# Performance work log

Measured on AMD Instinct MI355X. Metric: run time of the kernel, lower is better.

The kernel has to match this reference:

```python
import jax, jax.numpy as jnp
import numpy as np

B, S, E, H = 2, 2048, 1024, 16
DH = E // H  # 64


def setup_inputs() -> dict:
    key = jax.random.key(0)
    ks = jax.random.split(key, 10)
    scale = 1.0 / np.sqrt(E)
    x = jax.random.normal(ks[0], (B, S, E), dtype=jnp.float32)
    mask = jax.random.randint(ks[1], (B, S), 0, 2, dtype=jnp.int32)
    # per-head Q/K/V projections stacked: [H, E, DH] (x @ W, torch Linear transposed)
    wq = jax.random.normal(ks[2], (H, E, DH), dtype=jnp.float32) * scale
    wk = jax.random.normal(ks[3], (H, E, DH), dtype=jnp.float32) * scale
    wv = jax.random.normal(ks[4], (H, E, DH), dtype=jnp.float32) * scale
    bq = jax.random.normal(ks[5], (H, DH), dtype=jnp.float32) * scale
    bk = jax.random.normal(ks[6], (H, DH), dtype=jnp.float32) * scale
    bv = jax.random.normal(ks[7], (H, DH), dtype=jnp.float32) * scale
    wo = jax.random.normal(ks[8], (E, E), dtype=jnp.float32) * scale
    bo = jax.random.normal(ks[9], (E,), dtype=jnp.float32) * scale
    return {"x": x, "mask": mask, "wq": wq, "bq": bq, "wk": wk, "bk": bk,
            "wv": wv, "bv": bv, "wo": wo, "bo": bo}


def reference(x, mask, wq, bq, wk, bk, wv, bv, wo, bo):
    # q,k,v: [B, H, S, DH]
    q = jnp.einsum('bse,hed->bhsd', x, wq) + bq[None, :, None, :]
    k = jnp.einsum('bse,hed->bhsd', x, wk) + bk[None, :, None, :]
    v = jnp.einsum('bse,hed->bhsd', x, wv) + bv[None, :, None, :]
    scores = jnp.einsum('bhsd,bhtd->bhst', q, k) / np.sqrt(DH)
    # padding mask on key axis: mask==0 -> -1e9 (as in masked_fill)
    scores = jnp.where(mask[:, None, None, :] == 0, jnp.float32(-1e9), scores)
    attn = jax.nn.softmax(scores, axis=-1)
    o = jnp.einsum('bhst,bhtd->bhsd', attn, v)
    # concat heads -> [B, S, E], then output projection
    o = o.transpose(0, 2, 1, 3).reshape(B, S, E)
    return o @ wo + bo
```

## Files before the change

kernel.cpp:

```cpp
#include <hip/hip_runtime.h>
#include <hip/hip_bf16.h>
#include <math.h>

#define Bsz 2
#define Ssz 2048
#define Esz 1024
#define Hsz 16
#define DHsz 64

typedef __bf16 bf16_t;
typedef __attribute__((ext_vector_type(8))) __bf16 bf16x8;
typedef __attribute__((ext_vector_type(4))) float f32x4;

typedef unsigned int u32;
typedef const __attribute__((address_space(1))) u32* gptr_t;
typedef __attribute__((address_space(3))) u32* lptr_t;

#if __has_builtin(__builtin_amdgcn_exp2f)
#define EXP2F(x) __builtin_amdgcn_exp2f(x)
#else
#define EXP2F(x) __expf((x)*0.69314718f)
#endif

__device__ __forceinline__ bf16_t to_bf16(float f) {
  union { float f; unsigned u; } v; v.f = f;
  unsigned r = (v.u + 0x7FFF + ((v.u >> 16) & 1)) >> 16;
  union { unsigned short s; bf16_t b; } o; o.s = (unsigned short)r;
  return o.b;
}

__device__ __forceinline__ unsigned pack2_rtz(float a, float b) {
#if __has_builtin(__builtin_amdgcn_perm)
  return __builtin_amdgcn_perm(__float_as_uint(b), __float_as_uint(a), 0x07060302u);
#else
  return (__float_as_uint(a) >> 16) | (__float_as_uint(b) & 0xFFFF0000u);
#endif
}

__device__ __forceinline__ unsigned pack2(float a, float b) {
  union { float f; unsigned u; } x, y; x.f = a; y.f = b;
  unsigned ra = (x.u + 0x7FFF + ((x.u >> 16) & 1)) >> 16;
  unsigned rb = (y.u + 0x7FFF + ((y.u >> 16) & 1)) >> 16;
  return ra | (rb << 16);
}

__device__ __forceinline__ f32x4 mfma16(bf16x8 a, bf16x8 b, f32x4 c) {
  return __builtin_amdgcn_mfma_f32_16x16x32_bf16(a, b, c, 0, 0, 0);
}

__device__ __forceinline__ void gload16(void* lds, const void* g) {
  __builtin_amdgcn_global_load_lds((gptr_t)g, (lptr_t)lds, 16, 0, 0);
}

#define PREP_CAST 4096
#define PREP_MASK 4112
__global__ __launch_bounds__(256) void prep(
    const float* __restrict__ x, const int* __restrict__ mask,
    const float* __restrict__ wq, const float* __restrict__ wk,
    const float* __restrict__ wv, const float* __restrict__ wo,
    bf16_t* __restrict__ xb, bf16_t* __restrict__ mb,
    bf16_t* __restrict__ wAll, bf16_t* __restrict__ wAllV, bf16_t* __restrict__ woT) {
  __shared__ bf16_t lT[64 * 72];
  const int bid = blockIdx.x, t = threadIdx.x;
  if (bid < PREP_CAST) {
    const int i = bid * 256 + t;
    float4 v = ((const float4*)x)[i];
    uint2 o; o.x = pack2(v.x, v.y); o.y = pack2(v.z, v.w);
    ((uint2*)xb)[i] = o;
  } else if (bid < PREP_MASK) {
    const int i = (bid - PREP_CAST) * 256 + t;
    mb[i] = to_bf16(mask[i] ? 1.0f : 0.0f);
  } else {
    const int t2 = bid - PREP_MASK;
    const int et = t2 & 15, h = (t2 >> 4) & 15, z = t2 >> 8;
    const float* src; int srcLD; bf16_t* dst;
    if (z == 0)      { src = wq + ((size_t)h * Esz + et * 64) * DHsz; srcLD = DHsz; dst = wAll  + (size_t)(h * 64) * Esz; }
    else if (z == 1) { src = wk + ((size_t)h * Esz + et * 64) * DHsz; srcLD = DHsz; dst = wAll  + (size_t)(1024 + h * 64) * Esz; }
    else if (z == 2) { src = wv + ((size_t)h * Esz + et * 64) * DHsz; srcLD = DHsz; dst = wAllV + (size_t)(h * 64) * Esz; }
    else             { src = wo + (size_t)(et * 64) * Esz + h * 64;   srcLD = Esz;  dst = woT   + (size_t)(h * 64) * Esz; }
#pragma unroll
    for (int rr = 0; rr < 4; rr++) {
      int er = rr * 16 + (t >> 4);
      int dc = (t & 15) * 4;
      float4 v = *(const float4*)&src[(size_t)er * srcLD + dc];
      lT[(dc + 0) * 72 + er] = to_bf16(v.x);
      lT[(dc + 1) * 72 + er] = to_bf16(v.y);
      lT[(dc + 2) * 72 + er] = to_bf16(v.z);
      lT[(dc + 3) * 72 + er] = to_bf16(v.w);
    }
    __syncthreads();
#pragma unroll
    for (int rr = 0; rr < 2; rr++) {
      int d = rr * 32 + (t >> 3);
      int e8 = (t & 7) * 8;
      bf16x8 o = *(const bf16x8*)&lT[d * 72 + e8];
      *(bf16x8*)&dst[(size_t)d * Esz + et * 64 + e8] = o;
    }
  }
}

template <int TM, int TN>
__device__ __forceinline__ void gemm_core(
    const bf16_t* __restrict__ Ab, const bf16_t* __restrict__ Bb, int K,
    bf16_t* lA, bf16_t* lB, f32x4 (&acc)[TM / 32][TN / 32]) {
  const int tid = threadIdx.x, lane = tid & 63, wvi = tid >> 6;
  const int g = lane >> 4, c = lane & 15, cw = c & 7;
  const int lrow = lane >> 3, sg = lane & 7;
  const int wm = wvi >> 1, wn = wvi & 1;
  for (int kc = 0; kc < K; kc += 64) {
#pragma unroll
    for (int j = 0; j < TM / 32; j++) {
      const int base = (j * 4 + wvi) * 8;
      const int row = base + lrow;
      gload16(lA + base * 64, Ab + (size_t)row * K + kc + ((sg ^ (row & 7)) * 8));
    }
#pragma unroll
    for (int j = 0; j < TN / 32; j++) {
      const int base = (j * 4 + wvi) * 8;
      const int row = base + lrow;
      gload16(lB + base * 64, Bb + (size_t)row * K + kc + ((sg ^ (row & 7)) * 8));
    }
    __syncthreads();
#pragma unroll
    for (int ksp = 0; ksp < 2; ksp++) {
      const int kg = (ksp * 4 + g) ^ cw;
      bf16x8 af[TM / 32], bfr[TN / 32];
#pragma unroll
      for (int mt = 0; mt < TM / 32; mt++)
        af[mt] = *(const bf16x8*)&lA[(wm * (TM / 2) + mt * 16 + c) * 64 + kg * 8];
#pragma unroll
      for (int nt = 0; nt < TN / 32; nt++)
        bfr[nt] = *(const bf16x8*)&lB[(wn * (TN / 2) + nt * 16 + c) * 64 + kg * 8];
#pragma unroll
      for (int mt = 0; mt < TM / 32; mt++)
#pragma unroll
        for (int nt = 0; nt < TN / 32; nt++)
          acc[mt][nt] = mfma16(af[mt], bfr[nt], acc[mt][nt]);
    }
    __syncthreads();
  }
}

__global__ __launch_bounds__(256, 3) void qkv_gemm(
    const bf16_t* __restrict__ xb, const bf16_t* __restrict__ wAll,
    const bf16_t* __restrict__ wAllV, const bf16_t* __restrict__ mb,
    const float* __restrict__ bq, const float* __restrict__ bk,
    const float* __restrict__ bv,
    bf16_t* __restrict__ qb, bf16_t* __restrict__ kb, bf16_t* __restrict__ vTb) {
  __shared__ alignas(16) bf16_t lA[128 * 64];
  __shared__ alignas(16) bf16_t lB[128 * 64];
  const int bid = blockIdx.x;
  const int lane = threadIdx.x & 63, wvi = threadIdx.x >> 6;
  const int g = lane >> 4, c = lane & 15;
  const int wm = wvi >> 1, wn = wvi & 1;
  f32x4 acc[4][4] = {};
  if (bid < 512) {
    const int Mb = (bid & 31) * 128, Nb = (bid >> 5) * 128;
    gemm_core<128, 128>(xb + (size_t)Mb * Esz, wAll + (size_t)Nb * Esz, Esz, lA, lB, acc);
#pragma unroll
    for (int nt = 0; nt < 4; nt++) {
      const int col = Nb + wn * 64 + nt * 16 + c;
      const int which = col >> 10, h = (col >> 6) & 15, d = col & 63;
      const float bias = (which ? bk : bq)[h * DHsz + d];
      const float scale = which ? 1.0f : 0.18033688011112042f;
      bf16_t* dst = which ? kb : qb;
#pragma unroll
      for (int mt = 0; mt < 4; mt++)
#pragma unroll
        for (int r = 0; r < 4; r++) {
          const int row = Mb + wm * 64 + mt * 16 + g * 4 + r;
          const int b = row >> 11, s = row & 2047;
          dst[(((size_t)(b * Hsz + h)) * Ssz + s) * DHsz + d] =
              to_bf16((acc[mt][nt][r] + bias) * scale);
        }
    }
  } else {
    const int t2 = bid - 512;
    const int Mb = (t2 & 7) * 128, Nb = ((t2 >> 3) & 15) * 128, b = t2 >> 7;
    gemm_core<128, 128>(wAllV + (size_t)Mb * Esz, xb + ((size_t)(b * Ssz) + Nb) * Esz,
                        Esz, lA, lB, acc);
#pragma unroll
    for (int nt = 0; nt < 4; nt++) {
      const int s = Nb + wn * 64 + nt * 16 + c;
      const float mval = (float)mb[b * Ssz + s];
#pragma unroll
      for (int mt = 0; mt < 4; mt++)
#pragma unroll
        for (int r = 0; r < 4; r++) {
          const int m = Mb + wm * 64 + mt * 16 + g * 4 + r;
          vTb[((size_t)(b * 1024 + m)) * Ssz + s] = to_bf16((acc[mt][nt][r] + bv[m]) * mval);
        }
    }
  }
}

__global__ __launch_bounds__(128, 2) void flash_attn(
    const bf16_t* __restrict__ qb, const bf16_t* __restrict__ kb,
    const bf16_t* __restrict__ vTb, const bf16_t* __restrict__ mb,
    bf16_t* __restrict__ Ob) {
  __shared__ alignas(16) bf16_t lK[2][64 * 64];
  __shared__ alignas(16) bf16_t lP[2][32 * 64];

  const int h = blockIdx.x, qt = blockIdx.y, b = blockIdx.z;
  const size_t bh = (size_t)(b * Hsz + h);
  const int tid = threadIdx.x, lane = tid & 63, wv = tid >> 6;
  const int g = lane >> 4, c = lane & 15, cw = c & 7;
  const int lrow = lane >> 3, sg = lane & 7;

  const bf16_t* Kbase = kb + bh * (size_t)Ssz * DHsz;
  const bf16_t* Vlane = vTb + bh * (size_t)DHsz * Ssz + c * Ssz + g * 8;
  const bf16_t* mbb = mb + b * Ssz + g * 8;

  bf16x8 qf[2][2];
  const bf16_t* Qbase = qb + (bh * Ssz + qt * 64 + wv * 32) * DHsz;
#pragma unroll
  for (int qsub = 0; qsub < 2; qsub++)
#pragma unroll
    for (int ksp = 0; ksp < 2; ksp++)
      qf[qsub][ksp] = *(const bf16x8*)&Qbase[(qsub * 16 + c) * DHsz + ksp * 32 + g * 8];

  f32x4 o[2][4] = {};
  f32x4 lac[2] = {};

  auto stage = [&](int tc, int buf) {
#pragma unroll
    for (int j = 0; j < 4; j++) {
      const int rowbase = wv * 32 + j * 8;
      const int row = rowbase + lrow;
      const int lg = sg ^ (row & 7);
      gload16(&lK[buf][rowbase * 64], Kbase + ((size_t)(tc * 64 + row)) * DHsz + lg * 8);
    }
  };

  auto loadVM = [&](int tc, bf16x8 (&vf)[2][4], bf16x8 (&mfr)[2]) {
    const bf16_t* vp = Vlane + tc * 64;
#pragma unroll
    for (int ksp = 0; ksp < 2; ksp++) {
      mfr[ksp] = *(const bf16x8*)&mbb[tc * 64 + ksp * 32];
#pragma unroll
      for (int dt = 0; dt < 4; dt++)
        vf[ksp][dt] = *(const bf16x8*)&vp[dt * 16 * Ssz + ksp * 32];
    }
  };

  auto compute = [&](int buf, bf16x8 (&vf)[2][4], bf16x8 (&mfr)[2]) {
    const bf16_t* Kt = lK[buf];
    f32x4 st[2][4] = {};
#pragma unroll
    for (int ksp = 0; ksp < 2; ksp++) {
      const int kgr = (ksp * 4 + g) ^ cw;
#pragma unroll
      for (int nt = 0; nt < 4; nt++) {
        bf16x8 kf = *(const bf16x8*)&Kt[(nt * 16 + c) * 64 + kgr * 8];
        st[0][nt] = mfma16(kf, qf[0][ksp], st[0][nt]);
        st[1][nt] = mfma16(kf, qf[1][ksp], st[1][nt]);
      }
    }
#pragma unroll
    for (int qsub = 0; qsub < 2; qsub++)
#pragma unroll
      for (int nt = 0; nt < 4; nt++) {
        float p0 = EXP2F(st[qsub][nt][0]);
        float p1 = EXP2F(st[qsub][nt][1]);
        float p2 = EXP2F(st[qsub][nt][2]);
        float p3 = EXP2F(st[qsub][nt][3]);
        const int pg = (nt * 2 + (g >> 1)) ^ cw;
        uint2 pv; pv.x = pack2_rtz(p0, p1); pv.y = pack2_rtz(p2, p3);
        *(uint2*)&lP[wv][(qsub * 16 + c) * 64 + pg * 8 + (g & 1) * 4] = pv;
      }
#pragma unroll
    for (int ksp = 0; ksp < 2; ksp++) {
      const int kgr = (ksp * 4 + g) ^ cw;
      bf16x8 pf0 = *(const bf16x8*)&lP[wv][(0 * 16 + c) * 64 + kgr * 8];
      bf16x8 pf1 = *(const bf16x8*)&lP[wv][(1 * 16 + c) * 64 + kgr * 8];
      lac[0] = mfma16(pf0, mfr[ksp], lac[0]);
      lac[1] = mfma16(pf1, mfr[ksp], lac[1]);
#pragma unroll
      for (int dt = 0; dt < 4; dt++) {
        o[0][dt] = mfma16(pf0, vf[ksp][dt], o[0][dt]);
        o[1][dt] = mfma16(pf1, vf[ksp][dt], o[1][dt]);
      }
    }
  };

  bf16x8 vA[2][4], vB[2][4], mA[2], mB[2];
  stage(0, 0);
  loadVM(0, vA, mA);
  __syncthreads();
  for (int tc = 0; tc < 32; tc += 2) {
    stage(tc + 1, 1);
    loadVM(tc + 1, vB, mB);
    compute(0, vA, mA);
    __syncthreads();
    if (tc + 2 < 32) {
      stage(tc + 2, 0);
      loadVM(tc + 2, vA, mA);
    }
    compute(1, vB, mB);
    __syncthreads();
  }

#pragma unroll
  for (int qsub = 0; qsub < 2; qsub++)
#pragma unroll
    for (int r = 0; r < 4; r++) {
      const int row = qsub * 16 + g * 4 + r;
      const float linv = 1.0f / fmaxf(lac[qsub][r], 1e-30f);
      const size_t orow = (size_t)(b * Ssz + qt * 64 + wv * 32 + row) * Esz + h * DHsz;
#pragma unroll
      for (int dt = 0; dt < 4; dt++)
        Ob[orow + dt * 16 + c] = to_bf16(o[qsub][dt][r] * linv);
    }
}

__global__ __launch_bounds__(256, 3) void out_gemm(
    const bf16_t* __restrict__ Ob, const bf16_t* __restrict__ woT,
    const float* __restrict__ bo, float* __restrict__ out) {
  __shared__ alignas(16) bf16_t lA[128 * 64];
  __shared__ alignas(16) bf16_t lB[64 * 64];
  f32x4 acc[4][2] = {};
  const int Mb = blockIdx.x * 128, Nb = blockIdx.y * 64;
  gemm_core<128, 64>(Ob + (size_t)Mb * Esz, woT + (size_t)Nb * Esz, Esz, lA, lB, acc);
  const int lane = threadIdx.x & 63, wvi = threadIdx.x >> 6;
  const int g = lane >> 4, c = lane & 15;
  const int wm = wvi >> 1, wn = wvi & 1;
#pragma unroll
  for (int nt = 0; nt < 2; nt++) {
    const int col = Nb + wn * 32 + nt * 16 + c;
    const float bias = bo[col];
#pragma unroll
    for (int mt = 0; mt < 4; mt++)
#pragma unroll
      for (int r = 0; r < 4; r++) {
        const int row = Mb + wm * 64 + mt * 16 + g * 4 + r;
        out[(size_t)row * Esz + col] = acc[mt][nt][r] + bias;
      }
  }
}

extern "C" void kernel_launch(void* const* d_in, const int* in_sizes, int n_in,
                              void* d_out, int out_size, void* d_ws, size_t ws_size,
                              hipStream_t stream) {
  const float* x = (const float*)d_in[0];
  const int* mask = (const int*)d_in[1];
  const float* wq = (const float*)d_in[2];
  const float* bq = (const float*)d_in[3];
  const float* wk = (const float*)d_in[4];
  const float* bk = (const float*)d_in[5];
  const float* wv = (const float*)d_in[6];
  const float* bv = (const float*)d_in[7];
  const float* wo = (const float*)d_in[8];
  const float* bo = (const float*)d_in[9];
  float* out = (float*)d_out;

  char* ws = (char*)d_ws;
  size_t off = 0;
  auto take = [&](size_t bytes) -> char* {
    char* p = ws + off;
    off += (bytes + 255) & ~(size_t)255;
    return p;
  };
  bf16_t* xb    = (bf16_t*)take((size_t)Bsz * Ssz * Esz * 2);
  bf16_t* wAll  = (bf16_t*)take((size_t)2 * Esz * Esz * 2);
  bf16_t* wAllV = (bf16_t*)take((size_t)Esz * Esz * 2);
  bf16_t* woT   = (bf16_t*)take((size_t)Esz * Esz * 2);
  bf16_t* qb    = (bf16_t*)take((size_t)Bsz * Hsz * Ssz * DHsz * 2);
  bf16_t* kb    = (bf16_t*)take((size_t)Bsz * Hsz * Ssz * DHsz * 2);
  bf16_t* vTb   = (bf16_t*)take((size_t)Bsz * Hsz * Ssz * DHsz * 2);
  bf16_t* Ob    = (bf16_t*)take((size_t)Bsz * Ssz * Esz * 2);
  bf16_t* mb    = (bf16_t*)take((size_t)Bsz * Ssz * 2);

  prep<<<5136, 256, 0, stream>>>(x, mask, wq, wk, wv, wo, xb, mb, wAll, wAllV, woT);
  qkv_gemm<<<768, 256, 0, stream>>>(xb, wAll, wAllV, mb, bq, bk, bv, qb, kb, vTb);
  flash_attn<<<dim3(Hsz, Ssz / 64, Bsz), 128, 0, stream>>>(qb, kb, vTb, mb, Ob);
  out_gemm<<<dim3(Bsz * Ssz / 128, Esz / 64), 256, 0, stream>>>(Ob, woT, bo, out);
}
```

Measured before the change: 211.2 us.

## Split flash attention key range across two wave pairs and merge partials in LDS

The flash attention block grows from 128 to 256 threads. Two wave pairs each process half of the key sequence for the same 64 query rows, with separate K staging buffers, and the number of loop iterations is halved. The second pair writes its partial output and row-sum accumulators to LDS, and the first pair adds them in before normalizing and storing. The aim is more waves per block and shorter serial loops per wave, so latency is hidden better. The cost is more LDS, an extra barrier and merge step, and a higher launch-bounds occupancy target that may limit registers.

```diff
diff --git a/kernel.cpp b/kernel.cpp
--- a/kernel.cpp
+++ b/kernel.cpp
@@ -194,25 +194,26 @@
   }
 }
 
-__global__ __launch_bounds__(128, 2) void flash_attn(
+__global__ __launch_bounds__(256, 3) void flash_attn(
     const bf16_t* __restrict__ qb, const bf16_t* __restrict__ kb,
     const bf16_t* __restrict__ vTb, const bf16_t* __restrict__ mb,
     bf16_t* __restrict__ Ob) {
-  __shared__ alignas(16) bf16_t lK[2][64 * 64];
-  __shared__ alignas(16) bf16_t lP[2][32 * 64];
+  __shared__ alignas(16) bf16_t lK[2][2][64 * 64];
+  __shared__ alignas(16) bf16_t lP[4][32 * 64];
 
   const int h = blockIdx.x, qt = blockIdx.y, b = blockIdx.z;
   const size_t bh = (size_t)(b * Hsz + h);
   const int tid = threadIdx.x, lane = tid & 63, wv = tid >> 6;
+  const int qh = wv & 1, kh = wv >> 1;
   const int g = lane >> 4, c = lane & 15, cw = c & 7;
   const int lrow = lane >> 3, sg = lane & 7;
 
-  const bf16_t* Kbase = kb + bh * (size_t)Ssz * DHsz;
-  const bf16_t* Vlane = vTb + bh * (size_t)DHsz * Ssz + c * Ssz + g * 8;
-  const bf16_t* mbb = mb + b * Ssz + g * 8;
+  const bf16_t* Kbase = kb + bh * (size_t)Ssz * DHsz + (size_t)kh * 1024 * DHsz;
+  const bf16_t* Vlane = vTb + bh * (size_t)DHsz * Ssz + c * Ssz + g * 8 + kh * 1024;
+  const bf16_t* mbb = mb + b * Ssz + g * 8 + kh * 1024;
 
   bf16x8 qf[2][2];
-  const bf16_t* Qbase = qb + (bh * Ssz + qt * 64 + wv * 32) * DHsz;
+  const bf16_t* Qbase = qb + (bh * Ssz + qt * 64 + qh * 32) * DHsz;
 #pragma unroll
   for (int qsub = 0; qsub < 2; qsub++)
 #pragma unroll
@@ -225,10 +226,10 @@
   auto stage = [&](int tc, int buf) {
 #pragma unroll
     for (int j = 0; j < 4; j++) {
-      const int rowbase = wv * 32 + j * 8;
+      const int rowbase = qh * 32 + j * 8;
       const int row = rowbase + lrow;
       const int lg = sg ^ (row & 7);
-      gload16(&lK[buf][rowbase * 64], Kbase + ((size_t)(tc * 64 + row)) * DHsz + lg * 8);
+      gload16(&lK[kh][buf][rowbase * 64], Kbase + ((size_t)(tc * 64 + row)) * DHsz + lg * 8);
     }
   };
 
@@ -244,7 +245,7 @@
   };
 
   auto compute = [&](int buf, bf16x8 (&vf)[2][4], bf16x8 (&mfr)[2]) {
-    const bf16_t* Kt = lK[buf];
+    const bf16_t* Kt = lK[kh][buf];
     f32x4 st[2][4] = {};
 #pragma unroll
     for (int ksp = 0; ksp < 2; ksp++) {
@@ -287,12 +288,12 @@
   stage(0, 0);
   loadVM(0, vA, mA);
   __syncthreads();
-  for (int tc = 0; tc < 32; tc += 2) {
+  for (int tc = 0; tc < 16; tc += 2) {
     stage(tc + 1, 1);
     loadVM(tc + 1, vB, mB);
     compute(0, vA, mA);
     __syncthreads();
-    if (tc + 2 < 32) {
+    if (tc + 2 < 16) {
       stage(tc + 2, 0);
       loadVM(tc + 2, vA, mA);
     }
@@ -300,17 +301,38 @@
     __syncthreads();
   }
 
-#pragma unroll
-  for (int qsub = 0; qsub < 2; qsub++)
-#pragma unroll
-    for (int r = 0; r < 4; r++) {
-      const int row = qsub * 16 + g * 4 + r;
-      const float linv = 1.0f / fmaxf(lac[qsub][r], 1e-30f);
-      const size_t orow = (size_t)(b * Ssz + qt * 64 + wv * 32 + row) * Esz + h * DHsz;
+  float* mbuf = (float*)&lK[0][0][0];
+  float* slot = mbuf + (qh * 64 + lane) * 44;
+  if (kh) {
+#pragma unroll
+    for (int qsub = 0; qsub < 2; qsub++)
 #pragma unroll
       for (int dt = 0; dt < 4; dt++)
-        Ob[orow + dt * 16 + c] = to_bf16(o[qsub][dt][r] * linv);
-    }
+        *(f32x4*)&slot[qsub * 16 + dt * 4] = o[qsub][dt];
+    *(f32x4*)&slot[32] = lac[0];
+    *(f32x4*)&slot[36] = lac[1];
+  }
+  __syncthreads();
+  if (!kh) {
+#pragma unroll
+    for (int qsub = 0; qsub < 2; qsub++) {
+#pragma unroll
+      for (int dt = 0; dt < 4; dt++)
+        o[qsub][dt] += *(const f32x4*)&slot[qsub * 16 + dt * 4];
+      lac[qsub] += *(const f32x4*)&slot[32 + qsub * 4];
+    }
+#pragma unroll
+    for (int qsub = 0; qsub < 2; qsub++)
+#pragma unroll
+      for (int r = 0; r < 4; r++) {
+        const int row = qsub * 16 + g * 4 + r;
+        const float linv = 1.0f / fmaxf(lac[qsub][r], 1e-30f);
+        const size_t orow = (size_t)(b * Ssz + qt * 64 + qh * 32 + row) * Esz + h * DHsz;
+#pragma unroll
+        for (int dt = 0; dt < 4; dt++)
+          Ob[orow + dt * 16 + c] = to_bf16(o[qsub][dt][r] * linv);
+      }
+  }
 }
 
 __global__ __launch_bounds__(256, 3) void out_gemm(
@@ -372,6 +394,6 @@
 
   prep<<<5136, 256, 0, stream>>>(x, mask, wq, wk, wv, wo, xb, mb, wAll, wAllV, woT);
   qkv_gemm<<<768, 256, 0, stream>>>(xb, wAll, wAllV, mb, bq, bk, bv, qb, kb, vTb);
-  flash_attn<<<dim3(Hsz, Ssz / 64, Bsz), 128, 0, stream>>>(qb, kb, vTb, mb, Ob);
+  flash_attn<<<dim3(Hsz, Ssz / 64, Bsz), 256, 0, stream>>>(qb, kb, vTb, mb, Ob);
   out_gemm<<<dim3(Bsz * Ssz / 128, Esz / 64), 256, 0, stream>>>(Ob, woT, bo, out);
 }
```

Measured after the change: 302.7 us. 43.3% more time.

## Split flash attention into four waves of 16 query rows each

Applied to the files above, without the earlier changes.

Each flash-attention block now uses four waves, each handling 16 query rows instead of two waves with 32 rows each. The goal is to cut per-wave register pressure and raise occupancy and latency hiding. In exchange, each wave loads V and mask fragments and reads K from LDS for half as many rows, which doubles that traffic per unit of MFMA work.

```diff
diff --git a/kernel.cpp b/kernel.cpp
--- a/kernel.cpp
+++ b/kernel.cpp
@@ -194,12 +194,12 @@
   }
 }
 
-__global__ __launch_bounds__(128, 2) void flash_attn(
+__global__ __launch_bounds__(256, 4) void flash_attn(
     const bf16_t* __restrict__ qb, const bf16_t* __restrict__ kb,
     const bf16_t* __restrict__ vTb, const bf16_t* __restrict__ mb,
     bf16_t* __restrict__ Ob) {
   __shared__ alignas(16) bf16_t lK[2][64 * 64];
-  __shared__ alignas(16) bf16_t lP[2][32 * 64];
+  __shared__ alignas(16) bf16_t lP[4][16 * 64];
 
   const int h = blockIdx.x, qt = blockIdx.y, b = blockIdx.z;
   const size_t bh = (size_t)(b * Hsz + h);
@@ -211,21 +211,19 @@
   const bf16_t* Vlane = vTb + bh * (size_t)DHsz * Ssz + c * Ssz + g * 8;
   const bf16_t* mbb = mb + b * Ssz + g * 8;
 
-  bf16x8 qf[2][2];
-  const bf16_t* Qbase = qb + (bh * Ssz + qt * 64 + wv * 32) * DHsz;
-#pragma unroll
-  for (int qsub = 0; qsub < 2; qsub++)
-#pragma unroll
-    for (int ksp = 0; ksp < 2; ksp++)
-      qf[qsub][ksp] = *(const bf16x8*)&Qbase[(qsub * 16 + c) * DHsz + ksp * 32 + g * 8];
-
-  f32x4 o[2][4] = {};
-  f32x4 lac[2] = {};
+  bf16x8 qf[2];
+  const bf16_t* Qbase = qb + (bh * Ssz + qt * 64 + wv * 16) * DHsz;
+#pragma unroll
+  for (int ksp = 0; ksp < 2; ksp++)
+    qf[ksp] = *(const bf16x8*)&Qbase[c * DHsz + ksp * 32 + g * 8];
+
+  f32x4 o[4] = {};
+  f32x4 lac = {};
 
   auto stage = [&](int tc, int buf) {
 #pragma unroll
-    for (int j = 0; j < 4; j++) {
-      const int rowbase = wv * 32 + j * 8;
+    for (int j = 0; j < 2; j++) {
+      const int rowbase = wv * 16 + j * 8;
       const int row = rowbase + lrow;
       const int lg = sg ^ (row & 7);
       gload16(&lK[buf][rowbase * 64], Kbase + ((size_t)(tc * 64 + row)) * DHsz + lg * 8);
@@ -245,41 +243,34 @@
 
   auto compute = [&](int buf, bf16x8 (&vf)[2][4], bf16x8 (&mfr)[2]) {
     const bf16_t* Kt = lK[buf];
-    f32x4 st[2][4] = {};
+    f32x4 st[4] = {};
 #pragma unroll
     for (int ksp = 0; ksp < 2; ksp++) {
       const int kgr = (ksp * 4 + g) ^ cw;
 #pragma unroll
       for (int nt = 0; nt < 4; nt++) {
         bf16x8 kf = *(const bf16x8*)&Kt[(nt * 16 + c) * 64 + kgr * 8];
-        st[0][nt] = mfma16(kf, qf[0][ksp], st[0][nt]);
-        st[1][nt] = mfma16(kf, qf[1][ksp], st[1][nt]);
+        st[nt] = mfma16(kf, qf[ksp], st[nt]);
       }
     }
 #pragma unroll
-    for (int qsub = 0; qsub < 2; qsub++)
-#pragma unroll
-      for (int nt = 0; nt < 4; nt++) {
-        float p0 = EXP2F(st[qsub][nt][0]);
-        float p1 = EXP2F(st[qsub][nt][1]);
-        float p2 = EXP2F(st[qsub][nt][2]);
-        float p3 = EXP2F(st[qsub][nt][3]);
-        const int pg = (nt * 2 + (g >> 1)) ^ cw;
-        uint2 pv; pv.x = pack2_rtz(p0, p1); pv.y = pack2_rtz(p2, p3);
-        *(uint2*)&lP[wv][(qsub * 16 + c) * 64 + pg * 8 + (g & 1) * 4] = pv;
-      }
+    for (int nt = 0; nt < 4; nt++) {
+      float p0 = EXP2F(st[nt][0]);
+      float p1 = EXP2F(st[nt][1]);
+      float p2 = EXP2F(st[nt][2]);
+      float p3 = EXP2F(st[nt][3]);
+      const int pg = (nt * 2 + (g >> 1)) ^ cw;
+      uint2 pv; pv.x = pack2_rtz(p0, p1); pv.y = pack2_rtz(p2, p3);
+      *(uint2*)&lP[wv][c * 64 + pg * 8 + (g & 1) * 4] = pv;
+    }
 #pragma unroll
     for (int ksp = 0; ksp < 2; ksp++) {
       const int kgr = (ksp * 4 + g) ^ cw;
-      bf16x8 pf0 = *(const bf16x8*)&lP[wv][(0 * 16 + c) * 64 + kgr * 8];
-      bf16x8 pf1 = *(const bf16x8*)&lP[wv][(1 * 16 + c) * 64 + kgr * 8];
-      lac[0] = mfma16(pf0, mfr[ksp], lac[0]);
-      lac[1] = mfma16(pf1, mfr[ksp], lac[1]);
-#pragma unroll
-      for (int dt = 0; dt < 4; dt++) {
-        o[0][dt] = mfma16(pf0, vf[ksp][dt], o[0][dt]);
-        o[1][dt] = mfma16(pf1, vf[ksp][dt], o[1][dt]);
-      }
+      bf16x8 pf = *(const bf16x8*)&lP[wv][c * 64 + kgr * 8];
+      lac = mfma16(pf, mfr[ksp], lac);
+#pragma unroll
+      for (int dt = 0; dt < 4; dt++)
+        o[dt] = mfma16(pf, vf[ksp][dt], o[dt]);
     }
   };
 
@@ -301,16 +292,14 @@
   }
 
 #pragma unroll
-  for (int qsub = 0; qsub < 2; qsub++)
-#pragma unroll
-    for (int r = 0; r < 4; r++) {
-      const int row = qsub * 16 + g * 4 + r;
-      const float linv = 1.0f / fmaxf(lac[qsub][r], 1e-30f);
-      const size_t orow = (size_t)(b * Ssz + qt * 64 + wv * 32 + row) * Esz + h * DHsz;
-#pragma unroll
-      for (int dt = 0; dt < 4; dt++)
-        Ob[orow + dt * 16 + c] = to_bf16(o[qsub][dt][r] * linv);
-    }
+  for (int r = 0; r < 4; r++) {
+    const int row = g * 4 + r;
+    const float linv = 1.0f / fmaxf(lac[r], 1e-30f);
+    const size_t orow = (size_t)(b * Ssz + qt * 64 + wv * 16 + row) * Esz + h * DHsz;
+#pragma unroll
+    for (int dt = 0; dt < 4; dt++)
+      Ob[orow + dt * 16 + c] = to_bf16(o[dt][r] * linv);
+  }
 }
 
 __global__ __launch_bounds__(256, 3) void out_gemm(
@@ -372,6 +361,6 @@
 
   prep<<<5136, 256, 0, stream>>>(x, mask, wq, wk, wv, wo, xb, mb, wAll, wAllV, woT);
   qkv_gemm<<<768, 256, 0, stream>>>(xb, wAll, wAllV, mb, bq, bk, bv, qb, kb, vTb);
-  flash_attn<<<dim3(Hsz, Ssz / 64, Bsz), 128, 0, stream>>>(qb, kb, vTb, mb, Ob);
+  flash_attn<<<dim3(Hsz, Ssz / 64, Bsz), 256, 0, stream>>>(qb, kb, vTb, mb, Ob);
   out_gemm<<<dim3(Bsz * Ssz / 128, Esz / 64), 256, 0, stream>>>(Ob, woT, bo, out);
 }
```

Result: slower. 353.9 us (+67.5%).
